# Optimization experiments

Measured on AMD Instinct MI355X. Metric: run time of the kernel, lower is better.

The kernel has to match this reference:

```python
import jax, jax.numpy as jnp
import numpy as np
from functools import partial

B, C, H, W = 8, 12, 256, 256
N_CG = 11
CG_TOL = 1e-10

def conv(x, w, b):
    # NCHW conv, 3x3, stride 1, SAME padding
    y = jax.lax.conv_general_dilated(x, w, (1, 1), 'SAME',
                                     dimension_numbers=('NCHW', 'OIHW', 'NCHW'))
    return y + b[None, :, None, None]

def dw(x, params):
    (w1, b1, w2, b2, w3, b3, w4, b4, w5, b5) = params
    h = jax.nn.relu(conv(x, w1, b1))
    h = jax.nn.relu(conv(h, w2, b2))
    h = jax.nn.relu(conv(h, w3, b3))
    h = jax.nn.relu(conv(h, w4, b4))
    h = conv(h, w5, b5)
    return x + h  # residual shortcut

def myAtA(img, csm, mask, lam):
    # img: [B,H,W] complex; csm: [B,C,H,W] complex; mask: [B,H,W] real
    sf = jnp.sqrt(jnp.asarray(H * W, jnp.float32))
    coil = csm * img[:, None]                     # [B,C,H,W]
    ksp = jnp.fft.fft2(coil) / sf
    ksp = ksp * mask[:, None]
    ci = jnp.fft.ifft2(ksp) * sf
    return jnp.sum(ci * jnp.conj(csm), axis=1) + lam * img

def myCG(rhs, csm, mask, lam):
    x = jnp.zeros_like(rhs)
    r = rhs
    p = rhs
    rTr = jnp.sum(jnp.conj(r) * r).real.astype(jnp.float32)
    for _ in range(N_CG):  # fixed max iters, masked early-stop like host loop
        cont = rTr > CG_TOL
        Ap = myAtA(p, csm, mask, lam)
        denom = jnp.sum(jnp.conj(p) * Ap).real.astype(jnp.float32)
        denom_s = jnp.where(cont, denom, 1.0)
        alpha = (rTr / denom_s).astype(jnp.complex64)
        x_new = x + alpha * p
        r_new = r - alpha * Ap
        rTrNew = jnp.sum(jnp.conj(r_new) * r_new).real.astype(jnp.float32)
        beta = (rTrNew / jnp.where(cont, rTr, 1.0)).astype(jnp.complex64)
        p_new = r_new + beta * p
        x = jnp.where(cont, x_new, x)
        r = jnp.where(cont, r_new, r)
        p = jnp.where(cont, p_new, p)
        rTr = jnp.where(cont, rTrNew, rTr)
    return x

def setup_inputs() -> dict:
    key = jax.random.key(0)
    ks = jax.random.split(key, 16)
    inp = {
        'atb': jax.random.normal(ks[0], (B, 2, H, W), jnp.float32),
        'csm_real': jax.random.normal(ks[1], (B, C, H, W), jnp.float32) / np.sqrt(C),
        'csm_imag': jax.random.normal(ks[2], (B, C, H, W), jnp.float32) / np.sqrt(C),
        'mask': (jax.random.uniform(ks[3], (B, H, W)) < 0.33).astype(jnp.float32),
    }
    def xavier(k, shape):
        fan_in = shape[1] * shape[2] * shape[3]
        fan_out = shape[0] * shape[2] * shape[3]
        lim = np.sqrt(6.0 / (fan_in + fan_out))
        return jax.random.uniform(k, shape, jnp.float32, -lim, lim)
    inp['w1'] = xavier(ks[4], (64, 2, 3, 3)); inp['b1'] = jnp.zeros((64,), jnp.float32)
    inp['w2'] = xavier(ks[5], (64, 64, 3, 3)); inp['b2'] = jnp.zeros((64,), jnp.float32)
    inp['w3'] = xavier(ks[6], (64, 64, 3, 3)); inp['b3'] = jnp.zeros((64,), jnp.float32)
    inp['w4'] = xavier(ks[7], (64, 64, 3, 3)); inp['b4'] = jnp.zeros((64,), jnp.float32)
    inp['w5'] = xavier(ks[8], (2, 64, 3, 3)); inp['b5'] = jnp.zeros((2,), jnp.float32)
    inp['lam'] = jnp.asarray(0.05, jnp.float32)
    return inp

def reference(atb, csm_real, csm_imag, mask,
              w1, b1, w2, b2, w3, b3, w4, b4, w5, b5, lam):
    params = (w1, b1, w2, b2, w3, b3, w4, b4, w5, b5)
    out = dw(atb, params)                       # [B,2,H,W]
    rhs = atb + lam * out                       # [B,2,H,W]
    rhs_c = rhs[:, 0] + 1j * rhs[:, 1]          # r2c -> [B,H,W] complex
    csm = csm_real + 1j * csm_imag              # [B,C,H,W] complex
    x = myCG(rhs_c, csm, mask, lam.astype(jnp.complex64))
    return jnp.stack([x.real, x.imag], axis=1)  # c2r -> [B,2,H,W]
```

## Files before the change

kernel.cpp:

```cpp
#include <hip/hip_runtime.h>
#include <hip/hip_bf16.h>
#include <math.h>

static constexpr int NCOIL = 12;
static constexpr int HWSZ  = 65536;

typedef short v8s __attribute__((ext_vector_type(8)));
typedef float v4f __attribute__((ext_vector_type(4)));

__device__ __forceinline__ unsigned short f2bf(float v) {
  __hip_bfloat16 h = __float2bfloat16(v);
  union { __hip_bfloat16 h; unsigned short u; } cv; cv.h = h; return cv.u;
}
__device__ __forceinline__ float bf2f(unsigned short u) {
  return __uint_as_float(((unsigned)u) << 16);
}
__device__ __forceinline__ unsigned pack_bf(float2 v) {
  return ((unsigned)f2bf(v.y) << 16) | (unsigned)f2bf(v.x);
}
__device__ __forceinline__ float2 unpack_bf(unsigned u) {
  return make_float2(bf2f((unsigned short)(u & 0xffffu)),
                     bf2f((unsigned short)(u >> 16)));
}

__device__ __forceinline__ float2 cmulf(float2 a, float2 b) {
  return make_float2(a.x * b.x - a.y * b.y, a.x * b.y + a.y * b.x);
}
__device__ __forceinline__ float2 caddf(float2 a, float2 b) {
  return make_float2(a.x + b.x, a.y + b.y);
}
__device__ __forceinline__ float2 csubf(float2 a, float2 b) {
  return make_float2(a.x - b.x, a.y - b.y);
}

__device__ __forceinline__ float blockRed256(float v, float* sm) {
  #pragma unroll
  for (int off = 32; off; off >>= 1) v += __shfl_down(v, off);
  int lane = threadIdx.x & 63, wv = threadIdx.x >> 6;
  if (lane == 0) sm[wv] = v;
  __syncthreads();
  return sm[0] + sm[1] + sm[2] + sm[3];
}

__device__ __forceinline__ void blockRed2(float& a, float& b, float2* sm) {
  #pragma unroll
  for (int off = 32; off; off >>= 1) {
    a += __shfl_down(a, off);
    b += __shfl_down(b, off);
  }
  int lane = threadIdx.x & 63, wv = threadIdx.x >> 6;
  if (lane == 0) sm[wv] = make_float2(a, b);
  __syncthreads();
  float2 s0 = sm[0], s1 = sm[1], s2 = sm[2], s3 = sm[3];
  a = s0.x + s1.x + s2.x + s3.x;
  b = s0.y + s1.y + s2.y + s3.y;
}

__device__ __constant__ const float TC16[8] = {
  1.f, 0.92387953f, 0.70710678f, 0.38268343f, 0.f, -0.38268343f, -0.70710678f, -0.92387953f};
__device__ __constant__ const float TS16[8] = {
  0.f, -0.38268343f, -0.70710678f, -0.92387953f, -1.f, -0.92387953f, -0.70710678f, -0.38268343f};
__device__ __constant__ const int REV4[16] = {0,8,4,12,2,10,6,14,1,9,5,13,3,11,7,15};

template<int INV>
__device__ __forceinline__ void dif16(float2 v[16]) {
  #pragma unroll
  for (int ls = 0; ls < 4; ++ls) {
    const int len = 16 >> ls, half = len >> 1, step = 1 << ls;
    #pragma unroll
    for (int i = 0; i < 16; i += len) {
      #pragma unroll
      for (int j = 0; j < half; ++j) {
        float2 a = v[i + j], b = v[i + j + half];
        v[i + j] = caddf(a, b);
        float2 d = csubf(a, b);
        float cr = TC16[j * step];
        float ci = INV ? -TS16[j * step] : TS16[j * step];
        v[i + j + half] = make_float2(d.x * cr - d.y * ci, d.x * ci + d.y * cr);
      }
    }
  }
}

template<int INV>
__device__ __forceinline__ void dit16(float2 v[16]) {
  #pragma unroll
  for (int ls = 0; ls < 4; ++ls) {
    const int len = 2 << ls, half = len >> 1, step = 16 / len;
    #pragma unroll
    for (int i = 0; i < 16; i += len) {
      #pragma unroll
      for (int j = 0; j < half; ++j) {
        float cr = TC16[j * step];
        float ci = INV ? -TS16[j * step] : TS16[j * step];
        float2 b = v[i + j + half];
        float2 tt = make_float2(b.x * cr - b.y * ci, b.x * ci + b.y * cr);
        float2 a = v[i + j];
        v[i + j] = caddf(a, tt);
        v[i + j + half] = csubf(a, tt);
      }
    }
  }
}

__global__ __launch_bounds__(256) void k_prep(
    const float* __restrict__ w1, const float* __restrict__ w2,
    const float* __restrict__ w3, const float* __restrict__ w4,
    const float* __restrict__ w5, const float* __restrict__ csm_r,
    const float* __restrict__ csm_i,
    float* __restrict__ w1T, unsigned short* __restrict__ bf2,
    unsigned short* __restrict__ bf3, unsigned short* __restrict__ bf4,
    unsigned short* __restrict__ bf5, unsigned* __restrict__ csmh,
    float2* __restrict__ twf)
{
  const int bx = blockIdx.x;
  const int t = threadIdx.x;
  if (bx < 24576) {
    int i = bx * 256 + t;
    csmh[i] = ((unsigned)f2bf(csm_i[i]) << 16) | (unsigned)f2bf(csm_r[i]);
    return;
  }
  int r = bx - 24576;
  if (r < 432) {
    const float* w = (r < 144) ? w2 : (r < 288) ? w3 : w4;
    unsigned short* bf = (r < 144) ? bf2 : (r < 288) ? bf3 : bf4;
    int i = (r % 144) * 256 + t;
    int j = i & 7, lane = (i >> 3) & 63, ocg = (i >> 9) & 3, ks = i >> 11;
    int oc = (ocg << 4) + (lane & 15);
    int ic = ((ks & 1) << 5) + (((lane >> 4) & 3) << 3) + j;
    bf[i] = f2bf(w[(oc * 64 + ic) * 9 + (ks >> 1)]);
    return;
  }
  r -= 432;
  if (r < 36) {
    int i = r * 256 + t;
    int j = i & 7, lane = (i >> 3) & 63, ks = i >> 9;
    int oc = lane & 15;
    int ic = ((ks & 1) << 5) + (((lane >> 4) & 3) << 3) + j;
    bf5[i] = (oc < 2) ? f2bf(w5[(oc * 64 + ic) * 9 + (ks >> 1)]) : (unsigned short)0;
    return;
  }
  r -= 36;
  if (r < 5) {
    int i = r * 256 + t;
    if (i < 1152) {
      int oc = i & 63;
      int rest = i >> 6;
      int ic = rest / 9, k = rest - ic * 9;
      w1T[i] = w1[(oc * 2 + ic) * 9 + k];
    }
    return;
  }
  float ang = -6.28318530717958647692f * (float)t / 256.f;
  float s, c; sincosf(ang, &s, &c);
  twf[t] = make_float2(c, s);
}

__global__ __launch_bounds__(256) void k_conv1(
    const float* __restrict__ atb,
    const float* __restrict__ w1T,
    const float* __restrict__ b1,
    unsigned short* __restrict__ out)
{
  __shared__ float patch[2 * 324];
  const int t = threadIdx.x;
  const int img = blockIdx.z;
  const float* in = atb + (size_t)img * 131072;
  const int tx0 = blockIdx.x << 4, ty0 = blockIdx.y << 4;
  for (int i = t; i < 648; i += 256) {
    int ic = i / 324, rem = i - ic * 324;
    int py = rem / 18, px = rem - py * 18;
    int gy = ty0 + py - 1, gx = tx0 + px - 1;
    float v = 0.f;
    if ((unsigned)gy < 256u && (unsigned)gx < 256u)
      v = in[(ic << 16) + (gy << 8) + gx];
    patch[i] = v;
  }
  __syncthreads();
  const int tx = t & 15, ty = t >> 4;
  float acc[64];
  #pragma unroll
  for (int o = 0; o < 64; ++o) acc[o] = 0.f;
  #pragma unroll
  for (int ic = 0; ic < 2; ++ic) {
    const float* pb = &patch[ic * 324 + ty * 18 + tx];
    #pragma unroll
    for (int k = 0; k < 9; ++k) {
      const float v = pb[(k / 3) * 18 + (k % 3)];
      const float* wr = &w1T[(ic * 9 + k) << 6];
      #pragma unroll
      for (int o = 0; o < 64; ++o) acc[o] = fmaf(v, wr[o], acc[o]);
    }
  }
  size_t obase = ((size_t)img << 22) + ((size_t)(((ty0 + ty) << 8) + tx0 + tx) << 6);
  v8s* outv = (v8s*)(out + obase);
  #pragma unroll
  for (int g = 0; g < 8; ++g) {
    v8s ov;
    #pragma unroll
    for (int j = 0; j < 8; ++j) {
      float v = fmaxf(acc[(g << 3) + j] + b1[(g << 3) + j], 0.f);
      ov[j] = (short)f2bf(v);
    }
    outv[g] = ov;
  }
}

__global__ __launch_bounds__(256, 2) void k_conv_mfma(
    const unsigned short* __restrict__ in,
    const unsigned short* __restrict__ bfrag,
    const float* __restrict__ bias,
    unsigned short* __restrict__ out)
{
  __shared__ v8s halo[2592];
  __shared__ v8s bsh[2304];
  char* hb = (char*)halo;
  const int t = threadIdx.x;
  const int img = blockIdx.z;
  const int tx0 = blockIdx.x << 4, ty0 = blockIdx.y << 4;
  const size_t ibase = ((size_t)img << 22);
  for (int c = t; c < 2592; c += 256) {
    int hy = c / 144, rem = c - hy * 144;
    int hx = rem >> 3, slot = rem & 7;
    int gy = ty0 + hy - 1, gx = tx0 + hx - 1;
    v8s v = {0, 0, 0, 0, 0, 0, 0, 0};
    if ((unsigned)gy < 256u && (unsigned)gx < 256u)
      v = *(const v8s*)(in + ibase + ((size_t)((gy << 8) + gx) << 6) + (slot << 3));
    int xl = hy * 18 + hx;
    *(v8s*)(hb + xl * 128 + ((slot ^ (xl & 7)) << 4)) = v;
  }
  const v8s* bg = (const v8s*)bfrag;
  v8s breg[9];
  #pragma unroll
  for (int i = 0; i < 9; ++i) breg[i] = bg[t + (i << 8)];
  #pragma unroll
  for (int i = 0; i < 9; ++i) bsh[t + (i << 8)] = breg[i];
  #pragma unroll
  for (int i = 0; i < 9; ++i) breg[i] = bg[2304 + t + (i << 8)];
  __syncthreads();

  const int lane = t & 63, w = t >> 6;
  const int px = lane & 15, lg = lane >> 4;
  v4f acc[4][4];
  #pragma unroll
  for (int pf = 0; pf < 4; ++pf)
    #pragma unroll
    for (int og = 0; og < 4; ++og)
      #pragma unroll
      for (int rg = 0; rg < 4; ++rg) acc[pf][og][rg] = 0.f;

  #pragma unroll
  for (int half = 0; half < 2; ++half) {
    #pragma unroll
    for (int k9 = 0; k9 < 9; ++k9) {
      const int ks = half * 9 + k9;
      const int tap = ks >> 1;
      const int dy = tap / 3, dx = tap - dy * 3;
      const int slot = ((ks & 1) << 2) | lg;
      v8s b0 = bsh[((k9 << 2) | 0) * 64 + lane];
      v8s b1 = bsh[((k9 << 2) | 1) * 64 + lane];
      v8s b2 = bsh[((k9 << 2) | 2) * 64 + lane];
      v8s b3 = bsh[((k9 << 2) | 3) * 64 + lane];
      #pragma unroll
      for (int pf = 0; pf < 4; ++pf) {
        int xl = (w * 4 + pf + dy) * 18 + px + dx;
        v8s a = *(const v8s*)(hb + xl * 128 + ((slot ^ (xl & 7)) << 4));
        acc[pf][0] = __builtin_amdgcn_mfma_f32_16x16x32_bf16(a, b0, acc[pf][0], 0, 0, 0);
        acc[pf][1] = __builtin_amdgcn_mfma_f32_16x16x32_bf16(a, b1, acc[pf][1], 0, 0, 0);
        acc[pf][2] = __builtin_amdgcn_mfma_f32_16x16x32_bf16(a, b2, acc[pf][2], 0, 0, 0);
        acc[pf][3] = __builtin_amdgcn_mfma_f32_16x16x32_bf16(a, b3, acc[pf][3], 0, 0, 0);
      }
    }
    if (half == 0) {
      __syncthreads();
      #pragma unroll
      for (int i = 0; i < 9; ++i) bsh[t + (i << 8)] = breg[i];
      __syncthreads();
    }
  }
  const int ocl = lane & 15;
  float bv[4];
  #pragma unroll
  for (int og = 0; og < 4; ++og) bv[og] = bias[(og << 4) + ocl];
  #pragma unroll
  for (int pf = 0; pf < 4; ++pf) {
    const int gy = ty0 + (w << 2) + pf;
    #pragma unroll
    for (int og = 0; og < 4; ++og) {
      const int oc = (og << 4) + ocl;
      #pragma unroll
      for (int rg = 0; rg < 4; ++rg) {
        float v = fmaxf(acc[pf][og][rg] + bv[og], 0.f);
        int gx = tx0 + (lg << 2) + rg;
        out[ibase + ((size_t)((gy << 8) + gx) << 6) + oc] = f2bf(v);
      }
    }
  }
}

__global__ __launch_bounds__(512, 4) void k_conv5_rhs(
    const unsigned short* __restrict__ in,
    const unsigned short* __restrict__ bf5,
    const float* __restrict__ b5,
    const float* __restrict__ atb,
    const float* __restrict__ lam,
    float2* __restrict__ rhs)
{
  __shared__ v8s halo[2592];
  char* hb = (char*)halo;
  const int t = threadIdx.x;
  const int img = blockIdx.z;
  const int tx0 = blockIdx.x << 4, ty0 = blockIdx.y << 4;
  const size_t ibase = ((size_t)img << 22);
  for (int c = t; c < 2592; c += 512) {
    int hy = c / 144, rem = c - hy * 144;
    int hx = rem >> 3, slot = rem & 7;
    int gy = ty0 + hy - 1, gx = tx0 + hx - 1;
    v8s v = {0, 0, 0, 0, 0, 0, 0, 0};
    if ((unsigned)gy < 256u && (unsigned)gx < 256u)
      v = *(const v8s*)(in + ibase + ((size_t)((gy << 8) + gx) << 6) + (slot << 3));
    int xl = hy * 18 + hx;
    *(v8s*)(hb + xl * 128 + ((slot ^ (xl & 7)) << 4)) = v;
  }
  __syncthreads();
  const int lane = t & 63, w = t >> 6;
  const int px = lane & 15, lg = lane >> 4;
  v4f acc[2];
  #pragma unroll
  for (int pf = 0; pf < 2; ++pf)
    #pragma unroll
    for (int rg = 0; rg < 4; ++rg) acc[pf][rg] = 0.f;
  #pragma unroll
  for (int ks = 0; ks < 18; ++ks) {
    const int tap = ks >> 1;
    const int dy = tap / 3, dx = tap - dy * 3;
    const int slot = ((ks & 1) << 2) | lg;
    v8s b = *(const v8s*)(bf5 + (((ks * 64) + lane) << 3));
    #pragma unroll
    for (int pf = 0; pf < 2; ++pf) {
      int xl = (w * 2 + pf + dy) * 18 + px + dx;
      v8s a = *(const v8s*)(hb + xl * 128 + ((slot ^ (xl & 7)) << 4));
      acc[pf] = __builtin_amdgcn_mfma_f32_16x16x32_bf16(a, b, acc[pf], 0, 0, 0);
    }
  }
  const int ocl = lane & 15;
  const float l = *lam;
  const float bsel = b5[ocl & 1];
  #pragma unroll
  for (int pf = 0; pf < 2; ++pf) {
    const int gy = ty0 + w * 2 + pf;
    #pragma unroll
    for (int rg = 0; rg < 4; ++rg) {
      float v = acc[pf][rg] + bsel;
      float d1 = __shfl_down(v, 1);
      if (ocl == 0) {
        int gx = tx0 + (lg << 2) + rg;
        int pix = (gy << 8) + gx;
        float x0 = atb[(size_t)img * 131072 + pix];
        float x1 = atb[(size_t)img * 131072 + 65536 + pix];
        rhs[(size_t)img * 65536 + pix] =
            make_float2(fmaf(l, x0 + v, x0), fmaf(l, x1 + d1, x1));
      }
    }
  }
}

__global__ __launch_bounds__(256, 3) void k_coil_fft_rows(
    const float2* __restrict__ p_prev, const float2* __restrict__ r,
    float2* __restrict__ p_out,
    const float* __restrict__ part_r_old, const float* __restrict__ part_r_new,
    const int first,
    const unsigned* __restrict__ csmh, const float2* __restrict__ twf,
    unsigned* __restrict__ coil, float* __restrict__ part_p)
{
  __shared__ float2 trans[4096];
  __shared__ float2 sm2[4];
  __shared__ float sm1[4];
  const int t = threadIdx.x;
  const int b = blockIdx.x, cs = blockIdx.z;
  const int idx = t & 15, row16 = t >> 4;
  const int row = (blockIdx.y << 4) + row16;

  float beta = 0.f; bool do_upd = false;
  if (!first) {
    float so = 0.f, sn = 0.f;
    for (int i = t; i < 1024; i += 256) { so += part_r_old[i]; sn += part_r_new[i]; }
    blockRed2(so, sn, sm2);
    do_upd = so > 1e-10f;
    beta = do_upd ? sn / so : 0.f;
  }

  const int pb = (b << 16) + (row << 8);
  float2 pv[16];
  float pe = 0.f;
  #pragma unroll
  for (int h2 = 0; h2 < 16; ++h2) {
    int n = idx + (h2 << 4);
    float2 t0 = p_prev[pb + n];
    if (!first && do_upd) {
      float2 rv = r[pb + n];
      t0 = make_float2(fmaf(beta, t0.x, rv.x), fmaf(beta, t0.y, rv.y));
    }
    pv[h2] = t0;
    if (cs == 0) {
      if (!first) p_out[pb + n] = t0;
      pe = fmaf(t0.x, t0.x, fmaf(t0.y, t0.y, pe));
    }
  }
  if (cs == 0) {
    float tot = blockRed256(pe, sm1);
    if (t == 0) part_p[(b << 4) + blockIdx.y] = tot;
  }
  for (int j = 0; j < 2; ++j) {
    const int c = cs * 2 + j;
    const int gb = ((b * NCOIL + c) << 16) + (row << 8);
    float2 v[16];
    #pragma unroll
    for (int h2 = 0; h2 < 16; ++h2) {
      float2 cw = unpack_bf(csmh[gb + idx + (h2 << 4)]);
      v[h2] = cmulf(cw, pv[h2]);
    }
    dif16<0>(v);
    if (j) __syncthreads();
    #pragma unroll
    for (int rr = 0; rr < 16; ++rr) {
      int k1 = REV4[rr];
      v[rr] = cmulf(v[rr], twf[idx * k1]);
      trans[(k1 << 8) + (row16 << 4) + (idx ^ k1)] = v[rr];
    }
    __syncthreads();
    #pragma unroll
    for (int h1 = 0; h1 < 16; ++h1)
      v[h1] = trans[(idx << 8) + (row16 << 4) + (h1 ^ idx)];
    dif16<0>(v);
    #pragma unroll
    for (int rr = 0; rr < 16; ++rr)
      coil[gb + idx + (REV4[rr] << 4)] = pack_bf(v[rr]);
  }
}

__global__ __launch_bounds__(256) void k_fft_cols_mask(
    unsigned* __restrict__ coil, const float* __restrict__ mask,
    const float2* __restrict__ twf, float* __restrict__ part_m)
{
  __shared__ float2 trans[4096];
  __shared__ float smR[4];
  const int t = threadIdx.x;
  const int bc = blockIdx.x, b = bc / NCOIL;
  const int w0 = blockIdx.y << 4;
  const int col = t & 15, idx = t >> 4;
  const int base = (bc << 16) + w0 + col;
  float2 v[16];
  #pragma unroll
  for (int h2 = 0; h2 < 16; ++h2)
    v[h2] = unpack_bf(coil[base + ((idx + (h2 << 4)) << 8)]);
  dif16<0>(v);
  #pragma unroll
  for (int r = 0; r < 16; ++r) {
    int k1 = REV4[r];
    v[r] = cmulf(v[r], twf[idx * k1]);
    trans[(idx << 8) + (k1 << 4) + col] = v[r];
  }
  __syncthreads();
  #pragma unroll
  for (int h1 = 0; h1 < 16; ++h1)
    v[h1] = trans[(h1 << 8) + (idx << 4) + col];
  __syncthreads();
  dif16<0>(v);
  float pm = 0.f;
  #pragma unroll
  for (int r = 0; r < 16; ++r) {
    float mv = mask[(b << 16) + ((idx + (REV4[r] << 4)) << 8) + w0 + col];
    v[r].x *= mv; v[r].y *= mv;
    pm = fmaf(v[r].x, v[r].x, fmaf(v[r].y, v[r].y, pm));
  }
  float tot = blockRed256(pm, smR);
  if (t == 0) part_m[(bc << 4) + blockIdx.y] = tot;
  dit16<1>(v);
  #pragma unroll
  for (int r = 0; r < 16; ++r) {
    float2 w = twf[idx * r];
    v[r] = make_float2(v[r].x * w.x + v[r].y * w.y, v[r].y * w.x - v[r].x * w.y);
    trans[(idx << 8) + (r << 4) + col] = v[r];
  }
  __syncthreads();
  #pragma unroll
  for (int k1 = 0; k1 < 16; ++k1)
    v[k1] = trans[(k1 << 8) + (idx << 4) + col];
  dif16<1>(v);
  const float sc = 1.f / 256.f;
  #pragma unroll
  for (int r = 0; r < 16; ++r)
    coil[base + ((idx + (REV4[r] << 4)) << 8)] =
        pack_bf(make_float2(v[r].x * sc, v[r].y * sc));
}

__global__ __launch_bounds__(256) void k_ifft_rows_acc(
    const unsigned* __restrict__ coil, const unsigned* __restrict__ csmh,
    const float2* __restrict__ twf, unsigned* __restrict__ partbuf)
{
  __shared__ float2 trans[4096];
  const int t = threadIdx.x;
  const int b = blockIdx.x, cs = blockIdx.z;
  const int idx = t & 15, row16 = t >> 4;
  const int row = (blockIdx.y << 4) + row16;
  float2 acc[16];
  #pragma unroll
  for (int rr = 0; rr < 16; ++rr) acc[rr] = make_float2(0.f, 0.f);
  for (int j = 0; j < 3; ++j) {
    const int c = cs * 3 + j;
    const int gb = ((b * NCOIL + c) << 16) + (row << 8);
    float2 v[16];
    #pragma unroll
    for (int rr = 0; rr < 16; ++rr)
      v[rr] = unpack_bf(coil[gb + idx + (REV4[rr] << 4)]);
    dit16<1>(v);
    if (j) __syncthreads();
    #pragma unroll
    for (int rr = 0; rr < 16; ++rr) {
      float2 w = twf[idx * rr];
      float2 z = v[rr];
      trans[(rr << 8) + (row16 << 4) + (idx ^ rr)] =
          make_float2(z.x * w.x + z.y * w.y, z.y * w.x - z.x * w.y);
    }
    __syncthreads();
    #pragma unroll
    for (int k1 = 0; k1 < 16; ++k1)
      v[k1] = trans[(idx << 8) + (row16 << 4) + (k1 ^ idx)];
    dif16<1>(v);
    #pragma unroll
    for (int rr = 0; rr < 16; ++rr) {
      int gi = gb + idx + (REV4[rr] << 4);
      float2 cw = unpack_bf(csmh[gi]);
      float2 z = v[rr];
      acc[rr].x += cw.x * z.x + cw.y * z.y;
      acc[rr].y += cw.x * z.y - cw.y * z.x;
    }
  }
  const int ob = (((cs << 3) + b) << 16) + (row << 8);
  #pragma unroll
  for (int rr = 0; rr < 16; ++rr)
    partbuf[ob + idx + (REV4[rr] << 4)] = pack_bf(acc[rr]);
}

__global__ __launch_bounds__(256) void k_update1(
    float2* __restrict__ x, float2* __restrict__ r, const float2* __restrict__ p,
    const unsigned* __restrict__ partbuf,
    const float* __restrict__ part_m, const float* __restrict__ part_p,
    const float* __restrict__ part_r_old, float* __restrict__ part_r_new,
    const float* __restrict__ lam, float* __restrict__ outp)
{
  __shared__ float2 sm2[4];
  __shared__ float smA[4];
  __shared__ float smB[4];
  const int t = threadIdx.x;
  float se = 0.f, sp = 0.f, sr = 0.f;
  for (int i = t; i < 1536; i += 256) se += part_m[i];
  if (t < 128) sp = part_p[t];
  for (int i = t; i < 1024; i += 256) sr += part_r_old[i];
  blockRed2(se, sp, sm2);
  sr = blockRed256(sr, smA);
  const float l = *lam;
  const float denom = se * (1.f / 65536.f) + l * sp;
  const bool cont = sr > 1e-10f;
  const float alpha = cont ? sr / denom : 0.f;
  const float inv2 = 1.f / 256.f;
  float s = 0.f;
  #pragma unroll
  for (int e = 0; e < 2; ++e) {
    int pix = blockIdx.x * 512 + t + (e << 8);
    int b = pix >> 16, off = pix & 65535;
    float2 s0 = unpack_bf(partbuf[(b << 16) + off]);
    float2 s1 = unpack_bf(partbuf[((8 + b) << 16) + off]);
    float2 s2 = unpack_bf(partbuf[((16 + b) << 16) + off]);
    float2 s3 = unpack_bf(partbuf[((24 + b) << 16) + off]);
    float sx = (s0.x + s1.x) + (s2.x + s3.x);
    float sy = (s0.y + s1.y) + (s2.y + s3.y);
    float2 pv = p[pix], xv = x[pix], rv = r[pix];
    float2 apv = make_float2(fmaf(l, pv.x, sx * inv2), fmaf(l, pv.y, sy * inv2));
    xv.x = fmaf(alpha, pv.x, xv.x); xv.y = fmaf(alpha, pv.y, xv.y);
    rv.x = fmaf(-alpha, apv.x, rv.x); rv.y = fmaf(-alpha, apv.y, rv.y);
    x[pix] = xv; r[pix] = rv;
    if (outp) {
      outp[(b << 17) + off] = xv.x;
      outp[(b << 17) + 65536 + off] = xv.y;
    }
    s = fmaf(rv.x, rv.x, fmaf(rv.y, rv.y, s));
  }
  float tot = blockRed256(s, smB);
  if (t == 0) part_r_new[blockIdx.x] = tot;
}

__global__ __launch_bounds__(256) void k_cg_init(
    const float2* __restrict__ rhs, float2* __restrict__ x,
    float2* __restrict__ r, float2* __restrict__ p, float* __restrict__ part)
{
  __shared__ float sm[4];
  const int t = threadIdx.x;
  const int base = blockIdx.x * 512;
  float s = 0.f;
  #pragma unroll
  for (int e = 0; e < 2; ++e) {
    int idx = base + t + (e << 8);
    float2 v = rhs[idx];
    x[idx] = make_float2(0.f, 0.f);
    r[idx] = v; p[idx] = v;
    s = fmaf(v.x, v.x, fmaf(v.y, v.y, s));
  }
  float tot = blockRed256(s, sm);
  if (t == 0) part[blockIdx.x] = tot;
}

extern "C" void kernel_launch(void* const* d_in, const int* in_sizes, int n_in,
                              void* d_out, int out_size, void* d_ws, size_t ws_size,
                              hipStream_t stream) {
  (void)in_sizes; (void)n_in; (void)out_size; (void)ws_size;
  const float* atb   = (const float*)d_in[0];
  const float* csm_r = (const float*)d_in[1];
  const float* csm_i = (const float*)d_in[2];
  const float* mask  = (const float*)d_in[3];
  const float* w1 = (const float*)d_in[4];  const float* b1 = (const float*)d_in[5];
  const float* w2 = (const float*)d_in[6];  const float* b2 = (const float*)d_in[7];
  const float* w3 = (const float*)d_in[8];  const float* b3 = (const float*)d_in[9];
  const float* w4 = (const float*)d_in[10]; const float* b4 = (const float*)d_in[11];
  const float* w5 = (const float*)d_in[12]; const float* b5 = (const float*)d_in[13];
  const float* lam = (const float*)d_in[14];

  char* ws = (char*)d_ws;
  unsigned short* actA = (unsigned short*)ws;
  unsigned short* actB = (unsigned short*)(ws + 67108864);
  unsigned* coil   = (unsigned*)(ws + 134217728);
  unsigned* partbuf= (unsigned*)(ws + 159383552);
  float2* x        = (float2*)(ws + 176160768);
  float2* r        = (float2*)(ws + 180355072);
  float2* pbuf0    = (float2*)(ws + 184549376);
  float2* rhs      = (float2*)(ws + 188743680);
  float2* pbuf1    = rhs;
  unsigned* csmh   = (unsigned*)(ws + 192937984);
  float*  w1T      = (float*)(ws + 218103808);
  unsigned short* bf2 = (unsigned short*)(ws + 218108416);
  unsigned short* bf3 = (unsigned short*)(ws + 218182144);
  unsigned short* bf4 = (unsigned short*)(ws + 218255872);
  unsigned short* bf5 = (unsigned short*)(ws + 218329600);
  float2* twf      = (float2*)(ws + 218348032);
  float*  part_r   = (float*)(ws + 218350080);
  float*  part_m   = (float*)(ws + 218399232);
  float*  part_p   = (float*)(ws + 218405376);

  k_prep<<<25050, 256, 0, stream>>>(w1, w2, w3, w4, w5, csm_r, csm_i,
                                    w1T, bf2, bf3, bf4, bf5, csmh, twf);

  k_conv1<<<dim3(16, 16, 8), 256, 0, stream>>>(atb, w1T, b1, actA);
  k_conv_mfma<<<dim3(16, 16, 8), 256, 0, stream>>>(actA, bf2, b2, actB);
  k_conv_mfma<<<dim3(16, 16, 8), 256, 0, stream>>>(actB, bf3, b3, actA);
  k_conv_mfma<<<dim3(16, 16, 8), 256, 0, stream>>>(actA, bf4, b4, actB);
  k_conv5_rhs<<<dim3(16, 16, 8), 512, 0, stream>>>(actB, bf5, b5, atb, lam, rhs);

  k_cg_init<<<1024, 256, 0, stream>>>(rhs, x, r, pbuf0, part_r);
  for (int it = 0; it < 11; ++it) {
    float2* p_cur = (it % 2 == 0) ? pbuf0 : pbuf1;
    float2* p_prv = (it == 0) ? pbuf0 : ((it % 2 == 0) ? pbuf1 : pbuf0);
    const float* pro = part_r + (it > 0 ? (it - 1) : 0) * 1024;
    const float* prn = part_r + it * 1024;
    k_coil_fft_rows<<<dim3(8, 16, 6), 256, 0, stream>>>(
        p_prv, r, p_cur, pro, prn, it == 0 ? 1 : 0, csmh, twf, coil, part_p);
    k_fft_cols_mask<<<dim3(96, 16), 256, 0, stream>>>(coil, mask, twf, part_m);
    k_ifft_rows_acc<<<dim3(8, 16, 4), 256, 0, stream>>>(coil, csmh, twf, partbuf);
    k_update1<<<1024, 256, 0, stream>>>(x, r, p_cur, partbuf, part_m, part_p,
                                        part_r + it * 1024, part_r + (it + 1) * 1024, lam,
                                        it == 10 ? (float*)d_out : (float*)nullptr);
  }
}
```

Baseline: 921.7 us.

## Fuse inverse row FFT coil accumulation with CG x/r update kernel

Merges the inverse row-FFT/coil-combine kernel with the CG update kernel. Each block now handles 4 rows across all 12 coils, split into 4 coil groups of 3, and reduces the coil groups through shared memory. This removes the bf16 partbuf round trip to global memory and one kernel launch per iteration. The trade-off is fewer blocks (512 instead of 1024+512), which lowers parallelism, and the partial residual counts are resized to 512 to match.

```diff
diff --git a/kernel.cpp b/kernel.cpp
--- a/kernel.cpp
+++ b/kernel.cpp
@@ -384,7 +384,7 @@
   float beta = 0.f; bool do_upd = false;
   if (!first) {
     float so = 0.f, sn = 0.f;
-    for (int i = t; i < 1024; i += 256) { so += part_r_old[i]; sn += part_r_new[i]; }
+    for (int i = t; i < 512; i += 256) { so += part_r_old[i]; sn += part_r_new[i]; }
     blockRed2(so, sn, sm2);
     do_upd = so > 1e-10f;
     beta = do_upd ? sn / so : 0.f;
@@ -495,20 +495,39 @@
         pack_bf(make_float2(v[r].x * sc, v[r].y * sc));
 }
 
-__global__ __launch_bounds__(256) void k_ifft_rows_acc(
+__global__ __launch_bounds__(256) void k_ifft_rows_upd(
     const unsigned* __restrict__ coil, const unsigned* __restrict__ csmh,
-    const float2* __restrict__ twf, unsigned* __restrict__ partbuf)
+    const float2* __restrict__ twf,
+    const float2* __restrict__ p, float2* __restrict__ x, float2* __restrict__ r,
+    const float* __restrict__ part_m, const float* __restrict__ part_p,
+    const float* __restrict__ part_r_old, float* __restrict__ part_r_new,
+    const float* __restrict__ lam, float* __restrict__ outp)
 {
   __shared__ float2 trans[4096];
-  const int t = threadIdx.x;
-  const int b = blockIdx.x, cs = blockIdx.z;
-  const int idx = t & 15, row16 = t >> 4;
-  const int row = (blockIdx.y << 4) + row16;
+  __shared__ float2 sm2[4];
+  __shared__ float smA[4];
+  __shared__ float smB[4];
+  const int t = threadIdx.x;
+  const int b = blockIdx.x, rg = blockIdx.y;
+  const int cg = t >> 6, row4 = (t >> 4) & 3, idx = t & 15;
+  const int row = (rg << 2) + row4;
+
+  float se = 0.f, sp = 0.f, sr = 0.f;
+  for (int i = t; i < 1536; i += 256) se += part_m[i];
+  if (t < 128) sp = part_p[t];
+  for (int i = t; i < 512; i += 256) sr += part_r_old[i];
+  blockRed2(se, sp, sm2);
+  sr = blockRed256(sr, smA);
+  const float l = *lam;
+  const float denom = se * (1.f / 65536.f) + l * sp;
+  const float alpha = (sr > 1e-10f) ? sr / denom : 0.f;
+
   float2 acc[16];
   #pragma unroll
   for (int rr = 0; rr < 16; ++rr) acc[rr] = make_float2(0.f, 0.f);
+  const int tb = cg << 10;
   for (int j = 0; j < 3; ++j) {
-    const int c = cs * 3 + j;
+    const int c = cg * 3 + j;
     const int gb = ((b * NCOIL + c) << 16) + (row << 8);
     float2 v[16];
     #pragma unroll
@@ -520,13 +539,13 @@
     for (int rr = 0; rr < 16; ++rr) {
       float2 w = twf[idx * rr];
       float2 z = v[rr];
-      trans[(rr << 8) + (row16 << 4) + (idx ^ rr)] =
+      trans[tb + (rr << 6) + (row4 << 4) + (idx ^ rr)] =
           make_float2(z.x * w.x + z.y * w.y, z.y * w.x - z.x * w.y);
     }
     __syncthreads();
     #pragma unroll
     for (int k1 = 0; k1 < 16; ++k1)
-      v[k1] = trans[(idx << 8) + (row16 << 4) + (k1 ^ idx)];
+      v[k1] = trans[tb + (idx << 6) + (row4 << 4) + (k1 ^ idx)];
     dif16<1>(v);
     #pragma unroll
     for (int rr = 0; rr < 16; ++rr) {
@@ -537,50 +556,31 @@
       acc[rr].y += cw.x * z.y - cw.y * z.x;
     }
   }
-  const int ob = (((cs << 3) + b) << 16) + (row << 8);
-  #pragma unroll
-  for (int rr = 0; rr < 16; ++rr)
-    partbuf[ob + idx + (REV4[rr] << 4)] = pack_bf(acc[rr]);
-}
-
-__global__ __launch_bounds__(256) void k_update1(
-    float2* __restrict__ x, float2* __restrict__ r, const float2* __restrict__ p,
-    const unsigned* __restrict__ partbuf,
-    const float* __restrict__ part_m, const float* __restrict__ part_p,
-    const float* __restrict__ part_r_old, float* __restrict__ part_r_new,
-    const float* __restrict__ lam, float* __restrict__ outp)
-{
-  __shared__ float2 sm2[4];
-  __shared__ float smA[4];
-  __shared__ float smB[4];
-  const int t = threadIdx.x;
-  float se = 0.f, sp = 0.f, sr = 0.f;
-  for (int i = t; i < 1536; i += 256) se += part_m[i];
-  if (t < 128) sp = part_p[t];
-  for (int i = t; i < 1024; i += 256) sr += part_r_old[i];
-  blockRed2(se, sp, sm2);
-  sr = blockRed256(sr, smA);
-  const float l = *lam;
-  const float denom = se * (1.f / 65536.f) + l * sp;
-  const bool cont = sr > 1e-10f;
-  const float alpha = cont ? sr / denom : 0.f;
+  __syncthreads();
+  #pragma unroll
+  for (int rr = 0; rr < 16; ++rr) {
+    int c = idx + (REV4[rr] << 4);
+    trans[tb + (row4 << 8) + c] = acc[rr];
+  }
+  __syncthreads();
   const float inv2 = 1.f / 256.f;
   float s = 0.f;
   #pragma unroll
-  for (int e = 0; e < 2; ++e) {
-    int pix = blockIdx.x * 512 + t + (e << 8);
-    int b = pix >> 16, off = pix & 65535;
-    float2 s0 = unpack_bf(partbuf[(b << 16) + off]);
-    float2 s1 = unpack_bf(partbuf[((8 + b) << 16) + off]);
-    float2 s2 = unpack_bf(partbuf[((16 + b) << 16) + off]);
-    float2 s3 = unpack_bf(partbuf[((24 + b) << 16) + off]);
+  for (int e = 0; e < 4; ++e) {
+    int px = t + (e << 8);
+    float2 s0 = trans[px];
+    float2 s1 = trans[1024 + px];
+    float2 s2 = trans[2048 + px];
+    float2 s3 = trans[3072 + px];
     float sx = (s0.x + s1.x) + (s2.x + s3.x);
     float sy = (s0.y + s1.y) + (s2.y + s3.y);
-    float2 pv = p[pix], xv = x[pix], rv = r[pix];
-    float2 apv = make_float2(fmaf(l, pv.x, sx * inv2), fmaf(l, pv.y, sy * inv2));
-    xv.x = fmaf(alpha, pv.x, xv.x); xv.y = fmaf(alpha, pv.y, xv.y);
+    int off = (rg << 10) + px;
+    int gi = (b << 16) + off;
+    float2 pvv = p[gi], xv = x[gi], rv = r[gi];
+    float2 apv = make_float2(fmaf(l, pvv.x, sx * inv2), fmaf(l, pvv.y, sy * inv2));
+    xv.x = fmaf(alpha, pvv.x, xv.x); xv.y = fmaf(alpha, pvv.y, xv.y);
     rv.x = fmaf(-alpha, apv.x, rv.x); rv.y = fmaf(-alpha, apv.y, rv.y);
-    x[pix] = xv; r[pix] = rv;
+    x[gi] = xv; r[gi] = rv;
     if (outp) {
       outp[(b << 17) + off] = xv.x;
       outp[(b << 17) + 65536 + off] = xv.y;
@@ -588,7 +588,7 @@
     s = fmaf(rv.x, rv.x, fmaf(rv.y, rv.y, s));
   }
   float tot = blockRed256(s, smB);
-  if (t == 0) part_r_new[blockIdx.x] = tot;
+  if (t == 0) part_r_new[(b << 6) + rg] = tot;
 }
 
 __global__ __launch_bounds__(256) void k_cg_init(
@@ -597,10 +597,10 @@
 {
   __shared__ float sm[4];
   const int t = threadIdx.x;
-  const int base = blockIdx.x * 512;
+  const int base = blockIdx.x * 1024;
   float s = 0.f;
   #pragma unroll
-  for (int e = 0; e < 2; ++e) {
+  for (int e = 0; e < 4; ++e) {
     int idx = base + t + (e << 8);
     float2 v = rhs[idx];
     x[idx] = make_float2(0.f, 0.f);
@@ -630,7 +630,6 @@
   unsigned short* actA = (unsigned short*)ws;
   unsigned short* actB = (unsigned short*)(ws + 67108864);
   unsigned* coil   = (unsigned*)(ws + 134217728);
-  unsigned* partbuf= (unsigned*)(ws + 159383552);
   float2* x        = (float2*)(ws + 176160768);
   float2* r        = (float2*)(ws + 180355072);
   float2* pbuf0    = (float2*)(ws + 184549376);
@@ -644,8 +643,8 @@
   unsigned short* bf5 = (unsigned short*)(ws + 218329600);
   float2* twf      = (float2*)(ws + 218348032);
   float*  part_r   = (float*)(ws + 218350080);
-  float*  part_m   = (float*)(ws + 218399232);
-  float*  part_p   = (float*)(ws + 218405376);
+  float*  part_m   = (float*)(ws + 218374656);
+  float*  part_p   = (float*)(ws + 218380800);
 
   k_prep<<<25050, 256, 0, stream>>>(w1, w2, w3, w4, w5, csm_r, csm_i,
                                     w1T, bf2, bf3, bf4, bf5, csmh, twf);
@@ -656,18 +655,18 @@
   k_conv_mfma<<<dim3(16, 16, 8), 256, 0, stream>>>(actA, bf4, b4, actB);
   k_conv5_rhs<<<dim3(16, 16, 8), 512, 0, stream>>>(actB, bf5, b5, atb, lam, rhs);
 
-  k_cg_init<<<1024, 256, 0, stream>>>(rhs, x, r, pbuf0, part_r);
+  k_cg_init<<<512, 256, 0, stream>>>(rhs, x, r, pbuf0, part_r);
   for (int it = 0; it < 11; ++it) {
     float2* p_cur = (it % 2 == 0) ? pbuf0 : pbuf1;
     float2* p_prv = (it == 0) ? pbuf0 : ((it % 2 == 0) ? pbuf1 : pbuf0);
-    const float* pro = part_r + (it > 0 ? (it - 1) : 0) * 1024;
-    const float* prn = part_r + it * 1024;
+    const float* pro = part_r + (it > 0 ? (it - 1) : 0) * 512;
+    const float* prn = part_r + it * 512;
     k_coil_fft_rows<<<dim3(8, 16, 6), 256, 0, stream>>>(
         p_prv, r, p_cur, pro, prn, it == 0 ? 1 : 0, csmh, twf, coil, part_p);
     k_fft_cols_mask<<<dim3(96, 16), 256, 0, stream>>>(coil, mask, twf, part_m);
-    k_ifft_rows_acc<<<dim3(8, 16, 4), 256, 0, stream>>>(coil, csmh, twf, partbuf);
-    k_update1<<<1024, 256, 0, stream>>>(x, r, p_cur, partbuf, part_m, part_p,
-                                        part_r + it * 1024, part_r + (it + 1) * 1024, lam,
-                                        it == 10 ? (float*)d_out : (float*)nullptr);
-  }
-}
+    k_ifft_rows_upd<<<dim3(8, 64), 256, 0, stream>>>(
+        coil, csmh, twf, p_cur, x, r, part_m, part_p,
+        part_r + it * 512, part_r + (it + 1) * 512, lam,
+        it == 10 ? (float*)d_out : (float*)nullptr);
+  }
+}
```

New measurement: 852.1 us. -7.5%, faster.
